# Kernel tuning notes

Hardware: AMD Instinct MI355X
Metric: run time of the kernel (lower is better)

Reference implementation:

```python
import jax, jax.numpy as jnp
import numpy as np

N_USERS = 100000
N_MOVIES = 50000
H = 64
E = 2500000
L = 1000000
F_MOVIE = 20


def setup_inputs() -> dict:
    key = jax.random.key(0)
    ks = jax.random.split(key, 24)
    s = 0.1  # param init scale
    inp = {
        'user_node_id': jnp.arange(N_USERS, dtype=jnp.int64) if jax.config.jax_enable_x64 else jnp.arange(N_USERS, dtype=jnp.int32),
        'movie_node_id': jnp.arange(N_MOVIES, dtype=jnp.int32),
        'movie_x': jax.random.normal(ks[0], (N_MOVIES, F_MOVIE), jnp.float32),
        'edge_src_user': jax.random.randint(ks[1], (E,), 0, N_USERS),
        'edge_dst_movie': jax.random.randint(ks[2], (E,), 0, N_MOVIES),
        'eli_user': jax.random.randint(ks[3], (L,), 0, N_USERS),
        'eli_movie': jax.random.randint(ks[4], (L,), 0, N_MOVIES),
        # learned params
        'user_emb': jax.random.normal(ks[5], (N_USERS, H), jnp.float32) * s,
        'movie_emb': jax.random.normal(ks[6], (N_MOVIES, H), jnp.float32) * s,
        'lin_W': jax.random.normal(ks[7], (H, F_MOVIE), jnp.float32) * s,
        'lin_b': jnp.zeros((H,), jnp.float32),
    }
    # per layer (1,2) x per edge type (um: user->movie 'rates', mu: movie->user reverse)
    names = ['W1um_l', 'W1um_r', 'W1mu_l', 'W1mu_r', 'W2um_l', 'W2um_r', 'W2mu_l', 'W2mu_r']
    for i, n in enumerate(names):
        inp[n] = jax.random.normal(ks[8 + i], (H, H), jnp.float32) * s
    for i, n in enumerate(['b1um', 'b1mu', 'b2um', 'b2mu']):
        inp[n] = jnp.zeros((H,), jnp.float32)
    return inp


def _sage(x_src, x_dst, src, dst, n_dst, Wl, bl, Wr):
    # SAGEConv with mean aggregation: W_l @ mean_{j in N(i)} x_j + b + W_r @ x_i
    agg = jax.ops.segment_sum(x_src[src], dst, num_segments=n_dst)  # [n_dst, H]
    deg = jax.ops.segment_sum(jnp.ones((src.shape[0], 1), x_src.dtype), dst, num_segments=n_dst)
    mean = agg / jnp.maximum(deg, 1.0)
    return mean @ Wl.T + x_dst @ Wr.T + bl


def reference(user_node_id, movie_node_id, movie_x, edge_src_user, edge_dst_movie,
              eli_user, eli_movie, user_emb, movie_emb, lin_W, lin_b,
              W1um_l, W1um_r, W1mu_l, W1mu_r, W2um_l, W2um_r, W2mu_l, W2mu_r,
              b1um, b1mu, b2um, b2mu):
    # feature init
    x_user = user_emb[user_node_id]                                    # [U, H]
    x_movie = movie_x @ lin_W.T + lin_b + movie_emb[movie_node_id]     # [M, H]
    # layer 1 (hetero: one relation into each node type), then ReLU
    m1 = _sage(x_user, x_movie, edge_src_user, edge_dst_movie, N_MOVIES, W1um_l, b1um, W1um_r)
    u1 = _sage(x_movie, x_user, edge_dst_movie, edge_src_user, N_USERS, W1mu_l, b1mu, W1mu_r)
    x_user, x_movie = jax.nn.relu(u1), jax.nn.relu(m1)
    # layer 2 (no activation)
    m2 = _sage(x_user, x_movie, edge_src_user, edge_dst_movie, N_MOVIES, W2um_l, b2um, W2um_r)
    u2 = _sage(x_movie, x_user, edge_dst_movie, edge_src_user, N_USERS, W2mu_l, b2mu, W2mu_r)
    # edge dot-product classifier
    return (u2[eli_user] * m2[eli_movie]).sum(axis=-1)                 # [L]
```

## Files before the change

### kernel.cpp

```cpp
#include <hip/hip_runtime.h>
#include <hip/hip_fp16.h>

#define NU 100000
#define NM 50000
#define RM 4
#define RU 2
#define NBLK 256
#define NBKT 196
#define NH (NBKT * NBLK)
#define NKM (NM * RM)
#define NKU (NU * RU)

typedef __attribute__((ext_vector_type(8))) _Float16 f16x8;
typedef __attribute__((ext_vector_type(4))) float f32x4;

__device__ __forceinline__ unsigned pk2h(float a, float b) {
  return __builtin_bit_cast(unsigned, __floats2half2_rn(a, b));
}
__device__ __forceinline__ __half2 shfl_xor_h2(__half2 v, int m) {
  return __builtin_bit_cast(__half2, __shfl_xor(__builtin_bit_cast(int, v), m));
}

__global__ void k_scan_part(const int* __restrict__ cnt, int* __restrict__ off,
                            int* __restrict__ bsum, int n) {
  __shared__ int wsum[4];
  int t = threadIdx.x;
  int base = blockIdx.x * 1024 + t * 4;
  int v0 = (base + 0 < n) ? cnt[base + 0] : 0;
  int v1 = (base + 1 < n) ? cnt[base + 1] : 0;
  int v2 = (base + 2 < n) ? cnt[base + 2] : 0;
  int v3 = (base + 3 < n) ? cnt[base + 3] : 0;
  int s = v0 + v1 + v2 + v3;
  int lane = t & 63;
  int inc = s;
  #pragma unroll
  for (int d = 1; d < 64; d <<= 1) {
    int x = __shfl_up(inc, d);
    if (lane >= d) inc += x;
  }
  int wid = t >> 6;
  if (lane == 63) wsum[wid] = inc;
  __syncthreads();
  int woff = 0;
  for (int i = 0; i < wid; i++) woff += wsum[i];
  int excl = woff + inc - s;
  if (base + 0 < n) off[base + 0] = excl;
  if (base + 1 < n) off[base + 1] = excl + v0;
  if (base + 2 < n) off[base + 2] = excl + v0 + v1;
  if (base + 3 < n) off[base + 3] = excl + v0 + v1 + v2;
  if (t == 255) bsum[blockIdx.x] = woff + inc;
}

__global__ void k_scan_top(int* bsum, int nb) {
  int lane = threadIdx.x;
  int carry = 0;
  for (int base = 0; base < nb; base += 64) {
    int i = base + lane;
    int v = (i < nb) ? bsum[i] : 0;
    int inc = v;
    #pragma unroll
    for (int d = 1; d < 64; d <<= 1) {
      int x = __shfl_up(inc, d);
      if (lane >= d) inc += x;
    }
    if (i < nb) bsum[i] = carry + inc - v;
    carry += __shfl(inc, 63);
  }
}

__global__ void k_scan_add(int* __restrict__ off, const int* __restrict__ bsum,
                           int n, int total) {
  int i = blockIdx.x * blockDim.x + threadIdx.x;
  if (i < n) {
    off[i] = off[i] + bsum[i >> 10];
  } else if (i == n) {
    off[n] = total;
  }
}

__global__ void __launch_bounds__(256)
k_hist2(const int* __restrict__ esrc, const int* __restrict__ edst,
        int* __restrict__ hmat, int E) {
  __shared__ int hm[NBKT], hu[NBKT];
  int t = threadIdx.x;
  for (int b = t; b < NBKT; b += 256) { hm[b] = 0; hu[b] = 0; }
  __syncthreads();
  int chunk = (E + NBLK - 1) / NBLK;
  int beg = blockIdx.x * chunk;
  int end = min(beg + chunk, E);
  for (int e = beg + t; e < end; e += 256) {
    atomicAdd(&hm[edst[e] >> 8], 1);
    atomicAdd(&hu[esrc[e] >> 9], 1);
  }
  __syncthreads();
  for (int b = t; b < NBKT; b += 256) {
    hmat[b * NBLK + blockIdx.x] = hm[b];
    hmat[NH + b * NBLK + blockIdx.x] = hu[b];
  }
}

__global__ void __launch_bounds__(256)
k_part2(const int* __restrict__ esrc, const int* __restrict__ edst,
        const int* __restrict__ hbase, unsigned* __restrict__ rec_m,
        unsigned* __restrict__ rec_u, int E) {
  __shared__ int cm[NBKT], cu[NBKT];
  int t = threadIdx.x;
  for (int b = t; b < NBKT; b += 256) {
    cm[b] = hbase[b * NBLK + blockIdx.x];
    cu[b] = hbase[NH + b * NBLK + blockIdx.x] - E;
  }
  __syncthreads();
  int chunk = (E + NBLK - 1) / NBLK;
  int beg = blockIdx.x * chunk;
  int end = min(beg + chunk, E);
  for (int e = beg + t; e < end; e += 256) {
    int d = edst[e], s = esrc[e];
    unsigned lm = (unsigned)(d & 255) * RM + (unsigned)s / 25000u;
    int pm = atomicAdd(&cm[d >> 8], 1);
    rec_m[pm] = (lm << 17) | (unsigned)s;
    unsigned lu = (unsigned)(s & 511) * RU + (unsigned)d / 25000u;
    int pu = atomicAdd(&cu[s >> 9], 1);
    rec_u[pu] = (lu << 17) | (unsigned)d;
  }
}

__global__ void __launch_bounds__(256)
k_bcount2(const unsigned* __restrict__ rec_m, const unsigned* __restrict__ rec_u,
          const int* __restrict__ hbase, int* __restrict__ cnt, int E) {
  __shared__ int lcnt[1024];
  int b = blockIdx.x, t = threadIdx.x;
  bool mv = b < NBKT;
  int bb = mv ? b : b - NBKT;
  const unsigned* rec = mv ? rec_m : rec_u;
  int R = mv ? RM : RU, SH = mv ? 8 : 9, N = mv ? NM : NU;
  int* cntb = cnt + (mv ? 0 : NKM);
  int rs = mv ? hbase[bb * NBLK] : hbase[NH + bb * NBLK] - E;
  int re = mv ? hbase[(bb + 1) * NBLK] : hbase[NH + (bb + 1) * NBLK] - E;
  int node_lo = bb << SH;
  int wlen = (min(N - node_lo, 1 << SH)) * R;
  for (int i = t; i < wlen; i += 256) lcnt[i] = 0;
  __syncthreads();
  for (int r = rs + t; r < re; r += 256)
    atomicAdd(&lcnt[rec[r] >> 17], 1);
  __syncthreads();
  for (int i = t; i < wlen; i += 256) cntb[node_lo * R + i] = lcnt[i];
}

__global__ void __launch_bounds__(256)
k_bscatter2(const unsigned* __restrict__ rec_m, const unsigned* __restrict__ rec_u,
            const int* __restrict__ hbase, const int* __restrict__ off,
            int* __restrict__ nbr, int E) {
  __shared__ int lcur[1024];
  int b = blockIdx.x, t = threadIdx.x;
  bool mv = b < NBKT;
  int bb = mv ? b : b - NBKT;
  const unsigned* rec = mv ? rec_m : rec_u;
  int R = mv ? RM : RU, SH = mv ? 8 : 9, N = mv ? NM : NU;
  const int* offb = off + (mv ? 0 : NKM);
  int rs = mv ? hbase[bb * NBLK] : hbase[NH + bb * NBLK] - E;
  int re = mv ? hbase[(bb + 1) * NBLK] : hbase[NH + (bb + 1) * NBLK] - E;
  int node_lo = bb << SH;
  int wlen = (min(N - node_lo, 1 << SH)) * R;
  for (int i = t; i < wlen; i += 256) lcur[i] = offb[node_lo * R + i];
  __syncthreads();
  for (int r = rs + t; r < re; r += 256) {
    unsigned q = rec[r];
    int p = atomicAdd(&lcur[q >> 17], 1);
    nbr[p] = (int)(q & 0x1FFFFu);
  }
}

#define PREP_U 6250
#define PREP_M 12500
__global__ void __launch_bounds__(256)
k_prep(const float4* __restrict__ uemb4, unsigned short* __restrict__ uemb_h,
       const float* __restrict__ movie_x, const float* __restrict__ lin_W,
       const float* __restrict__ lin_b, const float* __restrict__ movie_emb,
       unsigned short* __restrict__ x_movie,
       const float* __restrict__ Wl0, const float* __restrict__ Wr0,
       const float* __restrict__ Wl1, const float* __restrict__ Wr1,
       const float* __restrict__ Wl2, const float* __restrict__ Wr2,
       const float* __restrict__ Wl3, const float* __restrict__ Wr3,
       unsigned short* __restrict__ Wc) {
  __shared__ float lwT[20 * 65];
  int b = blockIdx.x;
  if (b < PREP_U) {
    int i = b * 256 + threadIdx.x;
    float4 v = uemb4[i];
    uint2 o;
    o.x = pk2h(v.x, v.y);
    o.y = pk2h(v.z, v.w);
    *(uint2*)(uemb_h + (size_t)i * 4) = o;
  } else if (b < PREP_U + PREP_M) {
    int bb = b - PREP_U;
    for (int gidx = threadIdx.x; gidx < 64 * 20; gidx += 256) {
      int h = gidx / 20;
      int f = gidx - h * 20;
      lwT[f * 65 + h] = lin_W[gidx];
    }
    __syncthreads();
    int w = (bb * 256 + (int)threadIdx.x) >> 6;
    int h = threadIdx.x & 63;
    if (w >= NM) return;
    float acc = lin_b[h] + movie_emb[(size_t)w * 64 + h];
    const float* mx = movie_x + (size_t)w * 20;
    #pragma unroll
    for (int f = 0; f < 20; f++) acc += mx[f] * lwT[f * 65 + h];
    x_movie[(size_t)w * 64 + h] = __builtin_bit_cast(unsigned short, (__half)__float2half(acc));
  } else {
    int wb = b - PREP_U - PREP_M;
    int which = wb >> 5;
    const float* Wl = which == 0 ? Wl0 : which == 1 ? Wl1 : which == 2 ? Wl2 : Wl3;
    const float* Wr = which == 0 ? Wr0 : which == 1 ? Wr1 : which == 2 ? Wr2 : Wr3;
    int i = (wb & 31) * 256 + threadIdx.x;
    if (i >= 8192) return;
    int h = i >> 7, k = i & 127;
    float v = (k < 64) ? Wl[h * 64 + k] : Wr[h * 64 + (k - 64)];
    Wc[which * 8192 + i] = __builtin_bit_cast(unsigned short, (__half)__float2half(v));
  }
}

__global__ void __launch_bounds__(256)
k_gmean2(const unsigned short* __restrict__ xsrcM,
         const unsigned short* __restrict__ xsrcU,
         const int* __restrict__ nbr, const int* __restrict__ off,
         unsigned short* __restrict__ meanM, unsigned short* __restrict__ meanU) {
  int gw = (blockIdx.x * blockDim.x + threadIdx.x) >> 6;
  int lane = threadIdx.x & 63;
  if (gw >= NM + NU) return;
  bool mv = gw < NM;
  const unsigned short* xsrc = mv ? xsrcM : xsrcU;
  const int* offb = mv ? off : off + NKM;
  int w = mv ? gw : gw - NM;
  int R = mv ? RM : RU;
  unsigned short* meanT = mv ? meanM : meanU;
  int g = lane >> 3;
  int i = lane & 7;
  __half2 aa2[4];
  #pragma unroll
  for (int k = 0; k < 4; k++) aa2[k] = __builtin_bit_cast(__half2, 0u);

  int s0 = offb[w * R];
  int eN = offb[(w + 1) * R];
  for (int base = s0; base < eN; base += 32) {
    int cnw = eN - base;
    if (cnw > 32) cnw = 32;
    int lim = cnw - 1;
    int my = nbr[base + (lane < cnw ? lane : 0)];
    uint4 d0, d1, d2, d3;
    int j0 = __shfl(my, min(0 * 8 + g, lim));
    int j1 = __shfl(my, min(1 * 8 + g, lim));
    d0 = *(const uint4*)(xsrc + (size_t)j0 * 64 + i * 8);
    d1 = *(const uint4*)(xsrc + (size_t)j1 * 64 + i * 8);
    bool hi = cnw > 16;
    if (hi) {
      int j2 = __shfl(my, min(2 * 8 + g, lim));
      int j3 = __shfl(my, min(3 * 8 + g, lim));
      d2 = *(const uint4*)(xsrc + (size_t)j2 * 64 + i * 8);
      d3 = *(const uint4*)(xsrc + (size_t)j3 * 64 + i * 8);
    }
    #define CONSUME(dd, c)                                                    \
      {                                                                       \
        unsigned mcu = ((c) * 8 + g < cnw) ? 0x3C003C00u : 0u;                \
        __half2 mc2 = __builtin_bit_cast(__half2, mcu);                       \
        aa2[0] = __hfma2(__builtin_bit_cast(__half2, dd.x), mc2, aa2[0]);     \
        aa2[1] = __hfma2(__builtin_bit_cast(__half2, dd.y), mc2, aa2[1]);     \
        aa2[2] = __hfma2(__builtin_bit_cast(__half2, dd.z), mc2, aa2[2]);     \
        aa2[3] = __hfma2(__builtin_bit_cast(__half2, dd.w), mc2, aa2[3]);     \
      }
    CONSUME(d0, 0)
    CONSUME(d1, 1)
    if (hi) {
      CONSUME(d2, 2)
      CONSUME(d3, 3)
    }
    #undef CONSUME
  }
  #pragma unroll
  for (int m = 8; m <= 32; m <<= 1) {
    #pragma unroll
    for (int k = 0; k < 4; k++) aa2[k] = __hadd2(aa2[k], shfl_xor_h2(aa2[k], m));
  }
  float inv = 1.0f / fmaxf((float)(eN - s0), 1.0f);
  if (g == 0) {
    __half2 invh = __float2half2_rn(inv);
    uint4 o;
    o.x = __builtin_bit_cast(unsigned, __hmul2(aa2[0], invh));
    o.y = __builtin_bit_cast(unsigned, __hmul2(aa2[1], invh));
    o.z = __builtin_bit_cast(unsigned, __hmul2(aa2[2], invh));
    o.w = __builtin_bit_cast(unsigned, __hmul2(aa2[3], invh));
    *(uint4*)(meanT + ((size_t)w << 6) + i * 8) = o;
  }
}

template <int RELU>
__global__ void __launch_bounds__(256)
k_sage_gemm2(const unsigned short* __restrict__ meanM, const unsigned short* __restrict__ dvM,
             const unsigned short* __restrict__ WcM, const float* __restrict__ biasM,
             unsigned short* __restrict__ outM,
             const unsigned short* __restrict__ meanU, const unsigned short* __restrict__ dvU,
             const unsigned short* __restrict__ WcU, const float* __restrict__ biasU,
             unsigned short* __restrict__ outU) {
  __shared__ float ot[4][16][68];
  const int tM = NM / 16, tU = NU / 16;
  int wv4 = threadIdx.x >> 6;
  int wvg = (blockIdx.x * blockDim.x + threadIdx.x) >> 6;
  int lane = threadIdx.x & 63;
  bool active = wvg < tM + tU;
  bool mv = wvg < tM;
  const unsigned short* meanT = mv ? meanM : meanU;
  const unsigned short* dvT = mv ? dvM : dvU;
  const unsigned short* Wc = mv ? WcM : WcU;
  const float* bias = mv ? biasM : biasU;
  unsigned short* outT = mv ? outM : outU;
  int n0 = (mv ? wvg : wvg - tM) * 16;
  int rr = lane & 15;
  int ks = lane >> 4;

  if (active) {
    f16x8 bf[4][4];
    #pragma unroll
    for (int t = 0; t < 4; t++)
      #pragma unroll
      for (int kk = 0; kk < 4; kk++)
        bf[t][kk] = *(const f16x8*)(Wc + ((t * 16 + rr) << 7) + kk * 32 + ks * 8);
    f32x4 acc[4];
    #pragma unroll
    for (int t = 0; t < 4; t++) {
      float b = bias[t * 16 + rr];
      acc[t] = (f32x4){b, b, b, b};
    }
    const unsigned short* am = meanT + ((size_t)(n0 + rr) << 6);
    const unsigned short* ad = dvT + ((size_t)(n0 + rr) << 6);
    f16x8 af[4];
    af[0] = *(const f16x8*)(am + ks * 8);
    af[1] = *(const f16x8*)(am + 32 + ks * 8);
    af[2] = *(const f16x8*)(ad + ks * 8);
    af[3] = *(const f16x8*)(ad + 32 + ks * 8);
    #pragma unroll
    for (int kk = 0; kk < 4; kk++)
      #pragma unroll
      for (int t = 0; t < 4; t++)
        acc[t] = __builtin_amdgcn_mfma_f32_16x16x32_f16(af[kk], bf[t][kk], acc[t], 0, 0, 0);
    #pragma unroll
    for (int t = 0; t < 4; t++)
      #pragma unroll
      for (int r = 0; r < 4; r++) {
        float v = acc[t][r];
        if (RELU) v = fmaxf(v, 0.f);
        ot[wv4][(lane >> 4) * 4 + r][t * 16 + rr] = v;
      }
  }
  __syncthreads();
  if (active) {
    int nn = lane >> 2, c4 = lane & 3;
    const float* src = &ot[wv4][nn][c4 * 16];
    uint4 o0, o1;
    o0.x = pk2h(src[0], src[1]);  o0.y = pk2h(src[2], src[3]);
    o0.z = pk2h(src[4], src[5]);  o0.w = pk2h(src[6], src[7]);
    o1.x = pk2h(src[8], src[9]);  o1.y = pk2h(src[10], src[11]);
    o1.z = pk2h(src[12], src[13]); o1.w = pk2h(src[14], src[15]);
    unsigned short* dst = outT + ((size_t)(n0 + nn) << 6) + c4 * 16;
    *(uint4*)dst = o0;
    *(uint4*)(dst + 8) = o1;
  }
}

__global__ void __launch_bounds__(256)
k_dot(const unsigned short* __restrict__ u2, const unsigned short* __restrict__ m2,
      const int* __restrict__ eu, const int* __restrict__ em,
      float* __restrict__ out, int L) {
  int wave = (blockIdx.x * blockDim.x + threadIdx.x) >> 6;
  int lane = threadIdx.x & 63;
  int sub = lane & 15;
  int l = wave * 4 + (lane >> 4);
  int lc = l < L ? l : (L - 1);
  int iu = eu[lc], im = em[lc];
  uint2 a = *(const uint2*)(u2 + (size_t)iu * 64 + sub * 4);
  uint2 b = *(const uint2*)(m2 + (size_t)im * 64 + sub * 4);
  float2 a0 = __half22float2(__builtin_bit_cast(__half2, a.x));
  float2 a1 = __half22float2(__builtin_bit_cast(__half2, a.y));
  float2 b0 = __half22float2(__builtin_bit_cast(__half2, b.x));
  float2 b1 = __half22float2(__builtin_bit_cast(__half2, b.y));
  float s = a0.x * b0.x + a0.y * b0.y + a1.x * b1.x + a1.y * b1.y;
  s += __shfl_xor(s, 1);
  s += __shfl_xor(s, 2);
  s += __shfl_xor(s, 4);
  s += __shfl_xor(s, 8);
  if (sub == 0 && l < L) out[l] = s;
}

extern "C" void kernel_launch(void* const* d_in, const int* in_sizes, int n_in,
                              void* d_out, int out_size, void* d_ws, size_t ws_size,
                              hipStream_t stream) {
  const float* movie_x   = (const float*)d_in[2];
  const int*   esrc      = (const int*)d_in[3];
  const int*   edst      = (const int*)d_in[4];
  const int*   eli_u     = (const int*)d_in[5];
  const int*   eli_m     = (const int*)d_in[6];
  const float* user_emb  = (const float*)d_in[7];
  const float* movie_emb = (const float*)d_in[8];
  const float* lin_W     = (const float*)d_in[9];
  const float* lin_b     = (const float*)d_in[10];
  const float* W1um_l = (const float*)d_in[11];
  const float* W1um_r = (const float*)d_in[12];
  const float* W1mu_l = (const float*)d_in[13];
  const float* W1mu_r = (const float*)d_in[14];
  const float* W2um_l = (const float*)d_in[15];
  const float* W2um_r = (const float*)d_in[16];
  const float* W2mu_l = (const float*)d_in[17];
  const float* W2mu_r = (const float*)d_in[18];
  const float* b1um = (const float*)d_in[19];
  const float* b1mu = (const float*)d_in[20];
  const float* b2um = (const float*)d_in[21];
  const float* b2mu = (const float*)d_in[22];
  const int E = in_sizes[3];
  const int L = in_sizes[5];

  char* ws = (char*)d_ws;
  size_t o = 0;
  auto alloc = [&](size_t bytes) -> void* {
    void* p = ws + o;
    o = (o + bytes + 255) & ~(size_t)255;
    return p;
  };
  unsigned short* uemb_h   = (unsigned short*)alloc((size_t)NU * 64 * 2);
  unsigned short* xmovie_h = (unsigned short*)alloc((size_t)NM * 64 * 2);
  unsigned short* m1_h     = (unsigned short*)alloc((size_t)NM * 64 * 2);
  unsigned short* u1_h     = (unsigned short*)alloc((size_t)NU * 64 * 2);
  unsigned short* m2_h     = (unsigned short*)alloc((size_t)NM * 64 * 2);
  unsigned short* u2_h     = (unsigned short*)alloc((size_t)NU * 64 * 2);
  unsigned short* mean_m   = (unsigned short*)alloc((size_t)NM * 64 * 2);
  unsigned short* mean_u   = (unsigned short*)alloc((size_t)NU * 64 * 2);
  unsigned short* wcat     = (unsigned short*)alloc(4 * 8192 * 2);
  int* cnt   = (int*)alloc((size_t)(NKM + NKU) * 4);
  int* off   = (int*)alloc((size_t)(NKM + NKU + 1) * 4);
  int* bs    = (int*)alloc(4096);
  int* nbr   = (int*)alloc((size_t)2 * E * 4);
  int* hmat  = (int*)alloc((size_t)(2 * NH + 1) * 4);
  int* hbase = (int*)alloc((size_t)(2 * NH + 1) * 4);
  unsigned* rec_m = (unsigned*)uemb_h;
  unsigned* rec_u = (unsigned*)u1_h;

  k_hist2<<<NBLK, 256, 0, stream>>>(esrc, edst, hmat, E);
  {
    int n = 2 * NH, nb = (n + 1023) / 1024;
    k_scan_part<<<nb, 256, 0, stream>>>(hmat, hbase, bs, n);
    k_scan_top<<<1, 64, 0, stream>>>(bs, nb);
    k_scan_add<<<(n + 1 + 255) / 256, 256, 0, stream>>>(hbase, bs, n, 2 * E);
  }
  k_part2<<<NBLK, 256, 0, stream>>>(esrc, edst, hbase, rec_m, rec_u, E);
  k_bcount2<<<2 * NBKT, 256, 0, stream>>>(rec_m, rec_u, hbase, cnt, E);
  {
    int n = NKM + NKU, nb = (n + 1023) / 1024;
    k_scan_part<<<nb, 256, 0, stream>>>(cnt, off, bs, n);
    k_scan_top<<<1, 64, 0, stream>>>(bs, nb);
    k_scan_add<<<(n + 1 + 255) / 256, 256, 0, stream>>>(off, bs, n, 2 * E);
  }
  k_bscatter2<<<2 * NBKT, 256, 0, stream>>>(rec_m, rec_u, hbase, off, nbr, E);

  k_prep<<<PREP_U + PREP_M + 128, 256, 0, stream>>>(
      (const float4*)user_emb, uemb_h, movie_x, lin_W, lin_b, movie_emb, xmovie_h,
      W1um_l, W1um_r, W1mu_l, W1mu_r, W2um_l, W2um_r, W2mu_l, W2mu_r, wcat);
  unsigned short* wc1um = wcat;
  unsigned short* wc1mu = wcat + 8192;
  unsigned short* wc2um = wcat + 16384;
  unsigned short* wc2mu = wcat + 24576;

  int gGm = (NM + NU + 3) / 4;
  int gG = ((NM / 16 + NU / 16) + 3) / 4;
  k_gmean2<<<gGm, 256, 0, stream>>>(uemb_h, xmovie_h, nbr, off, mean_m, mean_u);
  k_sage_gemm2<1><<<gG, 256, 0, stream>>>(mean_m, xmovie_h, wc1um, b1um, m1_h,
                                          mean_u, uemb_h, wc1mu, b1mu, u1_h);
  k_gmean2<<<gGm, 256, 0, stream>>>(u1_h, m1_h, nbr, off, mean_m, mean_u);
  k_sage_gemm2<0><<<gG, 256, 0, stream>>>(mean_m, m1_h, wc2um, b2um, m2_h,
                                          mean_u, u1_h, wc2mu, b2mu, u2_h);

  k_dot<<<(L + 15) / 16, 256, 0, stream>>>(u2_h, m2_h, eli_u, eli_m, (float*)d_out, L);
}
```

Before: 375.1 us.

## Fuse bucket count, scan and scatter into one CSR build kernel

Merges the per-bucket count kernel, the global three-kernel scan and the scatter kernel into one kernel. Each block counts its bucket in shared memory, does a block-local scan offset by the bucket base, and scatters directly. This also emits per-node offsets instead of per-sub-key offsets. The gather-mean gets an unmasked fast path for full 32-neighbour chunks with 32-bit byte addressing. The dot kernel moves to 16-byte loads with 8 lanes per pair. Together these remove four launches and a global scan pass, at the cost of 32-bit offset arithmetic that assumes the buffers stay small.

```diff
diff --git a/kernel.cpp b/kernel.cpp
--- a/kernel.cpp
+++ b/kernel.cpp
@@ -8,8 +8,6 @@
 #define NBLK 256
 #define NBKT 196
 #define NH (NBKT * NBLK)
-#define NKM (NM * RM)
-#define NKU (NU * RU)
 
 typedef __attribute__((ext_vector_type(8))) _Float16 f16x8;
 typedef __attribute__((ext_vector_type(4))) float f32x4;
@@ -19,6 +17,9 @@
 }
 __device__ __forceinline__ __half2 shfl_xor_h2(__half2 v, int m) {
   return __builtin_bit_cast(__half2, __shfl_xor(__builtin_bit_cast(int, v), m));
+}
+__device__ __forceinline__ __half2 u2h2(unsigned v) {
+  return __builtin_bit_cast(__half2, v);
 }
 
 __global__ void k_scan_part(const int* __restrict__ cnt, int* __restrict__ off,
@@ -125,47 +126,58 @@
 }
 
 __global__ void __launch_bounds__(256)
-k_bcount2(const unsigned* __restrict__ rec_m, const unsigned* __restrict__ rec_u,
-          const int* __restrict__ hbase, int* __restrict__ cnt, int E) {
+k_bcsr(const unsigned* __restrict__ rec_m, const unsigned* __restrict__ rec_u,
+       const int* __restrict__ hbase, int* __restrict__ nbr,
+       int* __restrict__ nodeoffM, int* __restrict__ nodeoffU, int E) {
   __shared__ int lcnt[1024];
+  __shared__ int wsum[4];
   int b = blockIdx.x, t = threadIdx.x;
   bool mv = b < NBKT;
   int bb = mv ? b : b - NBKT;
   const unsigned* rec = mv ? rec_m : rec_u;
   int R = mv ? RM : RU, SH = mv ? 8 : 9, N = mv ? NM : NU;
-  int* cntb = cnt + (mv ? 0 : NKM);
+  int* nodeoff = mv ? nodeoffM : nodeoffU;
   int rs = mv ? hbase[bb * NBLK] : hbase[NH + bb * NBLK] - E;
   int re = mv ? hbase[(bb + 1) * NBLK] : hbase[NH + (bb + 1) * NBLK] - E;
+  int nbase = mv ? 0 : E;
   int node_lo = bb << SH;
-  int wlen = (min(N - node_lo, 1 << SH)) * R;
-  for (int i = t; i < wlen; i += 256) lcnt[i] = 0;
+  int node_hi = min(node_lo + (1 << SH), N);
+  for (int i = t; i < 1024; i += 256) lcnt[i] = 0;
   __syncthreads();
   for (int r = rs + t; r < re; r += 256)
     atomicAdd(&lcnt[rec[r] >> 17], 1);
   __syncthreads();
-  for (int i = t; i < wlen; i += 256) cntb[node_lo * R + i] = lcnt[i];
-}
-
-__global__ void __launch_bounds__(256)
-k_bscatter2(const unsigned* __restrict__ rec_m, const unsigned* __restrict__ rec_u,
-            const int* __restrict__ hbase, const int* __restrict__ off,
-            int* __restrict__ nbr, int E) {
-  __shared__ int lcur[1024];
-  int b = blockIdx.x, t = threadIdx.x;
-  bool mv = b < NBKT;
-  int bb = mv ? b : b - NBKT;
-  const unsigned* rec = mv ? rec_m : rec_u;
-  int R = mv ? RM : RU, SH = mv ? 8 : 9, N = mv ? NM : NU;
-  const int* offb = off + (mv ? 0 : NKM);
-  int rs = mv ? hbase[bb * NBLK] : hbase[NH + bb * NBLK] - E;
-  int re = mv ? hbase[(bb + 1) * NBLK] : hbase[NH + (bb + 1) * NBLK] - E;
-  int node_lo = bb << SH;
-  int wlen = (min(N - node_lo, 1 << SH)) * R;
-  for (int i = t; i < wlen; i += 256) lcur[i] = offb[node_lo * R + i];
+  int i0 = t * 4;
+  int v0 = lcnt[i0], v1 = lcnt[i0 + 1], v2 = lcnt[i0 + 2], v3 = lcnt[i0 + 3];
+  int s = v0 + v1 + v2 + v3;
+  int lane = t & 63;
+  int inc = s;
+  #pragma unroll
+  for (int d = 1; d < 64; d <<= 1) {
+    int x = __shfl_up(inc, d);
+    if (lane >= d) inc += x;
+  }
+  int wid = t >> 6;
+  if (lane == 63) wsum[wid] = inc;
+  __syncthreads();
+  int woff = 0;
+  for (int k = 0; k < wid; k++) woff += wsum[k];
+  int p0 = nbase + rs + woff + inc - s;
+  int p1 = p0 + v0, p2 = p1 + v1, p3 = p2 + v2;
+  lcnt[i0] = p0; lcnt[i0 + 1] = p1; lcnt[i0 + 2] = p2; lcnt[i0 + 3] = p3;
+  if (R == 4) {
+    int node = node_lo + (i0 >> 2);
+    if (node < node_hi) nodeoff[node] = p0;
+  } else {
+    int node = node_lo + (i0 >> 1);
+    if (node < node_hi) nodeoff[node] = p0;
+    if (node + 1 < node_hi) nodeoff[node + 1] = p2;
+  }
+  if (t == 0) nodeoff[node_hi] = nbase + re;
   __syncthreads();
   for (int r = rs + t; r < re; r += 256) {
     unsigned q = rec[r];
-    int p = atomicAdd(&lcur[q >> 17], 1);
+    int p = atomicAdd(&lcnt[q >> 17], 1);
     nbr[p] = (int)(q & 0x1FFFFu);
   }
 }
@@ -223,50 +235,68 @@
 __global__ void __launch_bounds__(256)
 k_gmean2(const unsigned short* __restrict__ xsrcM,
          const unsigned short* __restrict__ xsrcU,
-         const int* __restrict__ nbr, const int* __restrict__ off,
+         const int* __restrict__ nbr,
+         const int* __restrict__ nodeoffM, const int* __restrict__ nodeoffU,
          unsigned short* __restrict__ meanM, unsigned short* __restrict__ meanU) {
   int gw = (blockIdx.x * blockDim.x + threadIdx.x) >> 6;
   int lane = threadIdx.x & 63;
   if (gw >= NM + NU) return;
   bool mv = gw < NM;
-  const unsigned short* xsrc = mv ? xsrcM : xsrcU;
-  const int* offb = mv ? off : off + NKM;
+  const char* xb = (const char*)(mv ? xsrcM : xsrcU);
+  const int* noff = mv ? nodeoffM : nodeoffU;
   int w = mv ? gw : gw - NM;
-  int R = mv ? RM : RU;
   unsigned short* meanT = mv ? meanM : meanU;
   int g = lane >> 3;
-  int i = lane & 7;
+  unsigned ib = (unsigned)(lane & 7) * 16;
   __half2 aa2[4];
   #pragma unroll
-  for (int k = 0; k < 4; k++) aa2[k] = __builtin_bit_cast(__half2, 0u);
-
-  int s0 = offb[w * R];
-  int eN = offb[(w + 1) * R];
-  for (int base = s0; base < eN; base += 32) {
-    int cnw = eN - base;
-    if (cnw > 32) cnw = 32;
-    int lim = cnw - 1;
-    int my = nbr[base + (lane < cnw ? lane : 0)];
+  for (int k = 0; k < 4; k++) aa2[k] = u2h2(0u);
+
+  int s0 = noff[w], eN = noff[w + 1];
+  int deg = eN - s0;
+  int base = s0;
+  for (int nf = deg >> 5; nf > 0; nf--, base += 32) {
+    int my = nbr[base + (lane & 31)];
+    int j0 = __shfl(my, 0 * 8 + g);
+    int j1 = __shfl(my, 1 * 8 + g);
+    int j2 = __shfl(my, 2 * 8 + g);
+    int j3 = __shfl(my, 3 * 8 + g);
+    uint4 d0 = *(const uint4*)(xb + ((unsigned)(j0 << 7) + ib));
+    uint4 d1 = *(const uint4*)(xb + ((unsigned)(j1 << 7) + ib));
+    uint4 d2 = *(const uint4*)(xb + ((unsigned)(j2 << 7) + ib));
+    uint4 d3 = *(const uint4*)(xb + ((unsigned)(j3 << 7) + ib));
+    #define ADD4(dd)                                   \
+      aa2[0] = __hadd2(aa2[0], u2h2(dd.x));            \
+      aa2[1] = __hadd2(aa2[1], u2h2(dd.y));            \
+      aa2[2] = __hadd2(aa2[2], u2h2(dd.z));            \
+      aa2[3] = __hadd2(aa2[3], u2h2(dd.w));
+    ADD4(d0) ADD4(d1) ADD4(d2) ADD4(d3)
+    #undef ADD4
+  }
+  int rem = eN - base;
+  if (rem > 0) {
+    int lim = rem - 1;
+    int my = nbr[base + (lane < rem ? lane : 0)];
     uint4 d0, d1, d2, d3;
     int j0 = __shfl(my, min(0 * 8 + g, lim));
     int j1 = __shfl(my, min(1 * 8 + g, lim));
-    d0 = *(const uint4*)(xsrc + (size_t)j0 * 64 + i * 8);
-    d1 = *(const uint4*)(xsrc + (size_t)j1 * 64 + i * 8);
-    bool hi = cnw > 16;
+    d0 = *(const uint4*)(xb + ((unsigned)(j0 << 7) + ib));
+    d1 = *(const uint4*)(xb + ((unsigned)(j1 << 7) + ib));
+    bool hi = rem > 16;
     if (hi) {
       int j2 = __shfl(my, min(2 * 8 + g, lim));
       int j3 = __shfl(my, min(3 * 8 + g, lim));
-      d2 = *(const uint4*)(xsrc + (size_t)j2 * 64 + i * 8);
-      d3 = *(const uint4*)(xsrc + (size_t)j3 * 64 + i * 8);
+      d2 = *(const uint4*)(xb + ((unsigned)(j2 << 7) + ib));
+      d3 = *(const uint4*)(xb + ((unsigned)(j3 << 7) + ib));
     }
-    #define CONSUME(dd, c)                                                    \
-      {                                                                       \
-        unsigned mcu = ((c) * 8 + g < cnw) ? 0x3C003C00u : 0u;                \
-        __half2 mc2 = __builtin_bit_cast(__half2, mcu);                       \
-        aa2[0] = __hfma2(__builtin_bit_cast(__half2, dd.x), mc2, aa2[0]);     \
-        aa2[1] = __hfma2(__builtin_bit_cast(__half2, dd.y), mc2, aa2[1]);     \
-        aa2[2] = __hfma2(__builtin_bit_cast(__half2, dd.z), mc2, aa2[2]);     \
-        aa2[3] = __hfma2(__builtin_bit_cast(__half2, dd.w), mc2, aa2[3]);     \
+    #define CONSUME(dd, c)                                              \
+      {                                                                 \
+        unsigned mcu = ((c) * 8 + g < rem) ? 0x3C003C00u : 0u;          \
+        __half2 mc2 = u2h2(mcu);                                        \
+        aa2[0] = __hfma2(u2h2(dd.x), mc2, aa2[0]);                      \
+        aa2[1] = __hfma2(u2h2(dd.y), mc2, aa2[1]);                      \
+        aa2[2] = __hfma2(u2h2(dd.z), mc2, aa2[2]);                      \
+        aa2[3] = __hfma2(u2h2(dd.w), mc2, aa2[3]);                      \
       }
     CONSUME(d0, 0)
     CONSUME(d1, 1)
@@ -281,7 +311,7 @@
     #pragma unroll
     for (int k = 0; k < 4; k++) aa2[k] = __hadd2(aa2[k], shfl_xor_h2(aa2[k], m));
   }
-  float inv = 1.0f / fmaxf((float)(eN - s0), 1.0f);
+  float inv = 1.0f / fmaxf((float)deg, 1.0f);
   if (g == 0) {
     __half2 invh = __float2half2_rn(inv);
     uint4 o;
@@ -289,7 +319,7 @@
     o.y = __builtin_bit_cast(unsigned, __hmul2(aa2[1], invh));
     o.z = __builtin_bit_cast(unsigned, __hmul2(aa2[2], invh));
     o.w = __builtin_bit_cast(unsigned, __hmul2(aa2[3], invh));
-    *(uint4*)(meanT + ((size_t)w << 6) + i * 8) = o;
+    *(uint4*)((char*)meanT + ((unsigned)(w << 7) + ib)) = o;
   }
 }
 
@@ -323,20 +353,20 @@
     for (int t = 0; t < 4; t++)
       #pragma unroll
       for (int kk = 0; kk < 4; kk++)
-        bf[t][kk] = *(const f16x8*)(Wc + ((t * 16 + rr) << 7) + kk * 32 + ks * 8);
+        bf[t][kk] = *(const f16x8*)((const char*)Wc + (unsigned)(((t * 16 + rr) << 8) + kk * 64 + ks * 16));
     f32x4 acc[4];
     #pragma unroll
     for (int t = 0; t < 4; t++) {
       float b = bias[t * 16 + rr];
       acc[t] = (f32x4){b, b, b, b};
     }
-    const unsigned short* am = meanT + ((size_t)(n0 + rr) << 6);
-    const unsigned short* ad = dvT + ((size_t)(n0 + rr) << 6);
+    const char* am = (const char*)meanT + (unsigned)((n0 + rr) << 7);
+    const char* ad = (const char*)dvT + (unsigned)((n0 + rr) << 7);
     f16x8 af[4];
-    af[0] = *(const f16x8*)(am + ks * 8);
-    af[1] = *(const f16x8*)(am + 32 + ks * 8);
-    af[2] = *(const f16x8*)(ad + ks * 8);
-    af[3] = *(const f16x8*)(ad + 32 + ks * 8);
+    af[0] = *(const f16x8*)(am + ks * 16);
+    af[1] = *(const f16x8*)(am + 64 + ks * 16);
+    af[2] = *(const f16x8*)(ad + ks * 16);
+    af[3] = *(const f16x8*)(ad + 64 + ks * 16);
     #pragma unroll
     for (int kk = 0; kk < 4; kk++)
       #pragma unroll
@@ -372,21 +402,21 @@
       float* __restrict__ out, int L) {
   int wave = (blockIdx.x * blockDim.x + threadIdx.x) >> 6;
   int lane = threadIdx.x & 63;
-  int sub = lane & 15;
-  int l = wave * 4 + (lane >> 4);
+  int sub = lane & 7;
+  int l = wave * 8 + (lane >> 3);
   int lc = l < L ? l : (L - 1);
   int iu = eu[lc], im = em[lc];
-  uint2 a = *(const uint2*)(u2 + (size_t)iu * 64 + sub * 4);
-  uint2 b = *(const uint2*)(m2 + (size_t)im * 64 + sub * 4);
-  float2 a0 = __half22float2(__builtin_bit_cast(__half2, a.x));
-  float2 a1 = __half22float2(__builtin_bit_cast(__half2, a.y));
-  float2 b0 = __half22float2(__builtin_bit_cast(__half2, b.x));
-  float2 b1 = __half22float2(__builtin_bit_cast(__half2, b.y));
-  float s = a0.x * b0.x + a0.y * b0.y + a1.x * b1.x + a1.y * b1.y;
+  uint4 a = *(const uint4*)((const char*)u2 + ((unsigned)(iu << 7) + sub * 16));
+  uint4 b = *(const uint4*)((const char*)m2 + ((unsigned)(im << 7) + sub * 16));
+  float2 a0 = __half22float2(u2h2(a.x)), b0 = __half22float2(u2h2(b.x));
+  float2 a1 = __half22float2(u2h2(a.y)), b1 = __half22float2(u2h2(b.y));
+  float2 a2 = __half22float2(u2h2(a.z)), b2 = __half22float2(u2h2(b.z));
+  float2 a3 = __half22float2(u2h2(a.w)), b3 = __half22float2(u2h2(b.w));
+  float s = a0.x * b0.x + a0.y * b0.y + a1.x * b1.x + a1.y * b1.y
+          + a2.x * b2.x + a2.y * b2.y + a3.x * b3.x + a3.y * b3.y;
   s += __shfl_xor(s, 1);
   s += __shfl_xor(s, 2);
   s += __shfl_xor(s, 4);
-  s += __shfl_xor(s, 8);
   if (sub == 0 && l < L) out[l] = s;
 }
 
@@ -433,8 +463,8 @@
   unsigned short* mean_m   = (unsigned short*)alloc((size_t)NM * 64 * 2);
   unsigned short* mean_u   = (unsigned short*)alloc((size_t)NU * 64 * 2);
   unsigned short* wcat     = (unsigned short*)alloc(4 * 8192 * 2);
-  int* cnt   = (int*)alloc((size_t)(NKM + NKU) * 4);
-  int* off   = (int*)alloc((size_t)(NKM + NKU + 1) * 4);
+  int* nodeoffM = (int*)alloc((size_t)(NM + 1) * 4);
+  int* nodeoffU = (int*)alloc((size_t)(NU + 1) * 4);
   int* bs    = (int*)alloc(4096);
   int* nbr   = (int*)alloc((size_t)2 * E * 4);
   int* hmat  = (int*)alloc((size_t)(2 * NH + 1) * 4);
@@ -450,14 +480,7 @@
     k_scan_add<<<(n + 1 + 255) / 256, 256, 0, stream>>>(hbase, bs, n, 2 * E);
   }
   k_part2<<<NBLK, 256, 0, stream>>>(esrc, edst, hbase, rec_m, rec_u, E);
-  k_bcount2<<<2 * NBKT, 256, 0, stream>>>(rec_m, rec_u, hbase, cnt, E);
-  {
-    int n = NKM + NKU, nb = (n + 1023) / 1024;
-    k_scan_part<<<nb, 256, 0, stream>>>(cnt, off, bs, n);
-    k_scan_top<<<1, 64, 0, stream>>>(bs, nb);
-    k_scan_add<<<(n + 1 + 255) / 256, 256, 0, stream>>>(off, bs, n, 2 * E);
-  }
-  k_bscatter2<<<2 * NBKT, 256, 0, stream>>>(rec_m, rec_u, hbase, off, nbr, E);
+  k_bcsr<<<2 * NBKT, 256, 0, stream>>>(rec_m, rec_u, hbase, nbr, nodeoffM, nodeoffU, E);
 
   k_prep<<<PREP_U + PREP_M + 128, 256, 0, stream>>>(
       (const float4*)user_emb, uemb_h, movie_x, lin_W, lin_b, movie_emb, xmovie_h,
@@ -469,12 +492,12 @@
 
   int gGm = (NM + NU + 3) / 4;
   int gG = ((NM / 16 + NU / 16) + 3) / 4;
-  k_gmean2<<<gGm, 256, 0, stream>>>(uemb_h, xmovie_h, nbr, off, mean_m, mean_u);
+  k_gmean2<<<gGm, 256, 0, stream>>>(uemb_h, xmovie_h, nbr, nodeoffM, nodeoffU, mean_m, mean_u);
   k_sage_gemm2<1><<<gG, 256, 0, stream>>>(mean_m, xmovie_h, wc1um, b1um, m1_h,
                                           mean_u, uemb_h, wc1mu, b1mu, u1_h);
-  k_gmean2<<<gGm, 256, 0, stream>>>(u1_h, m1_h, nbr, off, mean_m, mean_u);
+  k_gmean2<<<gGm, 256, 0, stream>>>(u1_h, m1_h, nbr, nodeoffM, nodeoffU, mean_m, mean_u);
   k_sage_gemm2<0><<<gG, 256, 0, stream>>>(mean_m, m1_h, wc2um, b2um, m2_h,
                                           mean_u, u1_h, wc2mu, b2mu, u2_h);
 
-  k_dot<<<(L + 15) / 16, 256, 0, stream>>>(u2_h, m2_h, eli_u, eli_m, (float*)d_out, L);
-}
+  k_dot<<<(L + 31) / 32, 256, 0, stream>>>(u2_h, m2_h, eli_u, eli_m, (float*)d_out, L);
+}
```

After: 344.6 us. 1.09x faster.
